# Performance work log

Measured on AMD Instinct MI355X. Metric: run time of the kernel, lower is better.

The kernel has to match this reference:

```python
import jax, jax.numpy as jnp
import numpy as np
import math

B, N, D_IN, D_MODEL, N_HEADS = 512, 1024, 8, 64, 4
SIG_DIM = D_IN + D_IN * D_IN  # sig_depth=2: 8 + 64 = 72


def setup_inputs() -> dict:
    key = jax.random.key(0)
    ks = jax.random.split(key, 16)
    s = 0.05
    inp = {
        "features": jax.random.normal(ks[0], (B, N, D_IN), dtype=jnp.float32),
        "W_sig": jax.random.normal(ks[1], (SIG_DIM, D_MODEL), dtype=jnp.float32) * s,
        "b_sig": jax.random.normal(ks[2], (D_MODEL,), dtype=jnp.float32) * s,
        "W_feat": jax.random.normal(ks[3], (D_IN + 1, D_MODEL), dtype=jnp.float32) * s,
        "b_feat": jax.random.normal(ks[4], (D_MODEL,), dtype=jnp.float32) * s,
        "W_q": jax.random.normal(ks[5], (D_MODEL, D_MODEL), dtype=jnp.float32) * s,
        "b_q": jax.random.normal(ks[6], (D_MODEL,), dtype=jnp.float32) * s,
        "W_k": jax.random.normal(ks[7], (D_MODEL, D_MODEL), dtype=jnp.float32) * s,
        "b_k": jax.random.normal(ks[8], (D_MODEL,), dtype=jnp.float32) * s,
        "W_v": jax.random.normal(ks[9], (D_MODEL, D_MODEL), dtype=jnp.float32) * s,
        "b_v": jax.random.normal(ks[10], (D_MODEL,), dtype=jnp.float32) * s,
        "W_o": jax.random.normal(ks[11], (D_MODEL, D_MODEL), dtype=jnp.float32) * s,
        "b_o": jax.random.normal(ks[12], (D_MODEL,), dtype=jnp.float32) * s,
        "W_out": jax.random.normal(ks[13], (D_MODEL, 1), dtype=jnp.float32) * s,
        "b_out": jax.random.normal(ks[14], (1,), dtype=jnp.float32) * s,
    }
    return inp


def reference(features, W_sig, b_sig, W_feat, b_feat, W_q, b_q, W_k, b_k,
              W_v, b_v, W_o, b_o, W_out, b_out):
    b, n, d = features.shape
    dm = W_sig.shape[1]
    dh = dm // N_HEADS
    dt = features.dtype

    # --- path signature (depth 2) for every prefix, via Chen/cumsum closed form ---
    # increments inc_t = f[t+1] - f[t], t = 0..n-2
    inc = features[:, 1:, :] - features[:, :-1, :]              # (b, n-1, d)
    # C_j = sum_{t<j} inc_t  (exclusive cumsum)
    C = jnp.cumsum(inc, axis=1) - inc                           # (b, n-1, d)
    # sum_{i<j} inc_i (x) inc_j, flattened row-major as in torch .view
    outer = (C[:, :, :, None] * inc[:, :, None, :]).reshape(b, n - 1, d * d)
    S2 = jnp.cumsum(outer, axis=1)                              # prefix k uses index k-1
    sig2 = jnp.concatenate([jnp.zeros((b, 1, d * d), dt), S2], axis=1)  # (b, n, d*d)
    sig1 = features - features[:, :1, :]                        # f[k] - f[0]
    sig = jnp.concatenate([sig1, sig2], axis=-1)                # (b, n, SIG_DIM)

    sig_feat = sig @ W_sig + b_sig                              # (b, n, dm)
    # step k=0 uses literal zeros (no projection, no bias) in the original
    sig_feat = sig_feat.at[:, 0, :].set(0.0)

    # --- cross-attn with single key/value: softmax weights are exactly 1 ---
    v = sig_feat @ W_v + b_v                                    # (b, n, dm)
    # deltas do not depend on the query path, so compute them first to break
    # the (vacuous) recurrence, then feed them back as prev_delta for q.
    deltas_pre = ((v @ W_o + b_o) @ W_out + b_out)[..., 0]      # (b, n)
    prev = jnp.concatenate([jnp.zeros((b, 1), dt), deltas_pre[:, :-1]], axis=1)

    x = jnp.concatenate([features, prev[:, :, None]], axis=-1) @ W_feat + b_feat
    q = x @ W_q + b_q
    k = sig_feat @ W_k + b_k

    qh = q.reshape(b, n, N_HEADS, dh)
    kh = k.reshape(b, n, N_HEADS, dh)
    vh = v.reshape(b, n, N_HEADS, dh)
    logits = (qh * kh).sum(-1, keepdims=True) / math.sqrt(dh)   # (b, n, H, 1)
    w = jax.nn.softmax(logits, axis=-1)                         # == 1 (single key)
    attn = (w * vh).reshape(b, n, dm)
    out = attn @ W_o + b_o
    deltas = (out @ W_out + b_out)[..., 0]                      # (b, n)
    return deltas
```

## Files before the change

kernel.cpp:

```cpp
#include <hip/hip_runtime.h>

#define NPOS 1024
#define D 8

__global__ void sig_prep(const float* __restrict__ W_sig, const float* __restrict__ b_sig,
                         const float* __restrict__ W_v,  const float* __restrict__ b_v,
                         const float* __restrict__ W_o,  const float* __restrict__ b_o,
                         const float* __restrict__ W_out,const float* __restrict__ b_out,
                         float* __restrict__ ws) {
    __shared__ float u1[64];
    __shared__ float u[64];
    const int tid = threadIdx.x;
    if (tid < 64) {
        float s = 0.f;
        for (int j = 0; j < 64; ++j) s += W_o[tid * 64 + j] * W_out[j];
        u1[tid] = s;
    }
    __syncthreads();
    if (tid < 64) {
        float s = 0.f;
        for (int j = 0; j < 64; ++j) s += W_v[tid * 64 + j] * u1[j];
        u[tid] = s;
    }
    __syncthreads();
    if (tid < 72) {
        float s = 0.f;
        for (int j = 0; j < 64; ++j) s += W_sig[tid * 64 + j] * u[j];
        ws[tid] = s;
    }
    if (tid == 72) {
        float c = b_out[0];
        for (int j = 0; j < 64; ++j) c += b_v[j] * u1[j] + b_o[j] * W_out[j];
        float dd = c;
        for (int j = 0; j < 64; ++j) dd += b_sig[j] * u[j];
        ws[72] = dd;
        ws[73] = c;
    }
}

__global__ __launch_bounds__(256) void sig_main(const float* __restrict__ feat,
                                                const float* __restrict__ ws,
                                                float* __restrict__ out) {
    __shared__ float w2s[64];
    __shared__ float w1s[8];
    __shared__ float wtot[4];

    const int tid = threadIdx.x;
    const int b   = blockIdx.x;

    if (tid < 64) w2s[tid] = ws[8 + tid];
    else if (tid < 72) w1s[tid - 64] = ws[tid - 64];
    const float dval = ws[72];
    const float cval = ws[73];

    const float* __restrict__ frow = feat + (size_t)b * NPOS * D;

    float f0[D];
    {
        float4 a0 = *reinterpret_cast<const float4*>(frow);
        float4 a1 = *reinterpret_cast<const float4*>(frow + 4);
        f0[0]=a0.x; f0[1]=a0.y; f0[2]=a0.z; f0[3]=a0.w;
        f0[4]=a1.x; f0[5]=a1.y; f0[6]=a1.z; f0[7]=a1.w;
    }

    const int a = tid * 4;
    float fp[D];
    {
        float4 p0 = *reinterpret_cast<const float4*>(frow + a * D);
        float4 p1 = *reinterpret_cast<const float4*>(frow + a * D + 4);
        fp[0]=p0.x; fp[1]=p0.y; fp[2]=p0.z; fp[3]=p0.w;
        fp[4]=p1.x; fp[5]=p1.y; fp[6]=p1.z; fp[7]=p1.w;
    }

    __syncthreads();

    float l[4];
    float dotv[4];
    float run = 0.f;
#pragma unroll
    for (int i = 0; i < 4; ++i) {
        const int s = a + i;
        float gi = 0.f;
        if (s < NPOS - 1) {
            float fn[D];
            float4 n0 = *reinterpret_cast<const float4*>(frow + (s + 1) * D);
            float4 n1 = *reinterpret_cast<const float4*>(frow + (s + 1) * D + 4);
            fn[0]=n0.x; fn[1]=n0.y; fn[2]=n0.z; fn[3]=n0.w;
            fn[4]=n1.x; fn[5]=n1.y; fn[6]=n1.z; fn[7]=n1.w;

            float inc[D];
#pragma unroll
            for (int k = 0; k < D; ++k) inc[k] = fn[k] - fp[k];
#pragma unroll
            for (int r = 0; r < D; ++r) {
                float acc = 0.f;
#pragma unroll
                for (int j = 0; j < D; ++j) acc += w2s[r * D + j] * inc[j];
                gi += (fp[r] - f0[r]) * acc;
            }
            float dv = 0.f;
#pragma unroll
            for (int k = 0; k < D; ++k) dv += (fn[k] - f0[k]) * w1s[k];
            dotv[i] = dv;
#pragma unroll
            for (int k = 0; k < D; ++k) fp[k] = fn[k];
        } else {
            dotv[i] = 0.f;
        }
        run += gi;
        l[i] = run;
    }

    const int lane = tid & 63;
    const int wave = tid >> 6;
    float t = run;
#pragma unroll
    for (int off = 1; off < 64; off <<= 1) {
        float nv = __shfl_up(t, off);
        if (lane >= off) t += nv;
    }
    if (lane == 63) wtot[wave] = t;
    __syncthreads();
    float base = t - run;
#pragma unroll
    for (int w = 0; w < 4; ++w)
        if (w < wave) base += wtot[w];

    float* __restrict__ orow = out + (size_t)b * NPOS;
    if (tid == 0) orow[0] = cval;
#pragma unroll
    for (int i = 0; i < 4; ++i) {
        const int s = a + i;
        const int tpos = s + 1;
        if (tpos < NPOS) {
            orow[tpos] = dotv[i] + base + l[i] + dval;
        }
    }
}

extern "C" void kernel_launch(void* const* d_in, const int* in_sizes, int n_in,
                              void* d_out, int out_size, void* d_ws, size_t ws_size,
                              hipStream_t stream) {
    const float* features = (const float*)d_in[0];
    const float* W_sig    = (const float*)d_in[1];
    const float* b_sig    = (const float*)d_in[2];
    const float* W_v      = (const float*)d_in[9];
    const float* b_v      = (const float*)d_in[10];
    const float* W_o      = (const float*)d_in[11];
    const float* b_o      = (const float*)d_in[12];
    const float* W_out    = (const float*)d_in[13];
    const float* b_out    = (const float*)d_in[14];

    float* ws  = (float*)d_ws;
    float* out = (float*)d_out;

    sig_prep<<<1, 128, 0, stream>>>(W_sig, b_sig, W_v, b_v, W_o, b_o, W_out, b_out, ws);
    sig_main<<<512, 256, 0, stream>>>(features, ws, out);
}
```

Measured before the change: 98.49 us.

## Fuse weight-prep into main kernel and use one thread per position

Drops the separate single-block prep kernel and has every block recompute the collapsed weight vectors (W_o·W_out, W_v·u, W_sig·u) into shared memory, saving a launch and the serial dependency between the two kernels. The main kernel moves from 256 threads doing 4 positions each to 1024 threads doing one position each, with a 16-wave scan instead of a 4-wave one. The cost is redundant 64x64 matrix-vector work in all 512 blocks, three extra barriers, and larger blocks.

```diff
diff --git a/kernel.cpp b/kernel.cpp
--- a/kernel.cpp
+++ b/kernel.cpp
@@ -3,59 +3,39 @@
 #define NPOS 1024
 #define D 8
 
-__global__ void sig_prep(const float* __restrict__ W_sig, const float* __restrict__ b_sig,
-                         const float* __restrict__ W_v,  const float* __restrict__ b_v,
-                         const float* __restrict__ W_o,  const float* __restrict__ b_o,
-                         const float* __restrict__ W_out,const float* __restrict__ b_out,
-                         float* __restrict__ ws) {
+__global__ __launch_bounds__(1024) void sig_fused(
+    const float* __restrict__ feat,
+    const float* __restrict__ W_sig, const float* __restrict__ b_sig,
+    const float* __restrict__ W_v,   const float* __restrict__ b_v,
+    const float* __restrict__ W_o,   const float* __restrict__ b_o,
+    const float* __restrict__ W_out, const float* __restrict__ b_out,
+    float* __restrict__ out)
+{
     __shared__ float u1[64];
-    __shared__ float u[64];
-    const int tid = threadIdx.x;
-    if (tid < 64) {
-        float s = 0.f;
-        for (int j = 0; j < 64; ++j) s += W_o[tid * 64 + j] * W_out[j];
-        u1[tid] = s;
-    }
-    __syncthreads();
-    if (tid < 64) {
-        float s = 0.f;
-        for (int j = 0; j < 64; ++j) s += W_v[tid * 64 + j] * u1[j];
-        u[tid] = s;
-    }
-    __syncthreads();
-    if (tid < 72) {
-        float s = 0.f;
-        for (int j = 0; j < 64; ++j) s += W_sig[tid * 64 + j] * u[j];
-        ws[tid] = s;
-    }
-    if (tid == 72) {
-        float c = b_out[0];
-        for (int j = 0; j < 64; ++j) c += b_v[j] * u1[j] + b_o[j] * W_out[j];
-        float dd = c;
-        for (int j = 0; j < 64; ++j) dd += b_sig[j] * u[j];
-        ws[72] = dd;
-        ws[73] = c;
-    }
-}
-
-__global__ __launch_bounds__(256) void sig_main(const float* __restrict__ feat,
-                                                const float* __restrict__ ws,
-                                                float* __restrict__ out) {
+    __shared__ float uu[64];
     __shared__ float w2s[64];
     __shared__ float w1s[8];
-    __shared__ float wtot[4];
+    __shared__ float dc[2];
+    __shared__ float wtot[16];
 
     const int tid = threadIdx.x;
     const int b   = blockIdx.x;
-
-    if (tid < 64) w2s[tid] = ws[8 + tid];
-    else if (tid < 72) w1s[tid - 64] = ws[tid - 64];
-    const float dval = ws[72];
-    const float cval = ws[73];
-
     const float* __restrict__ frow = feat + (size_t)b * NPOS * D;
 
-    float f0[D];
+    float fs[D], fn[D], f0[D];
+    {
+        float4 a0 = *reinterpret_cast<const float4*>(frow + tid * D);
+        float4 a1 = *reinterpret_cast<const float4*>(frow + tid * D + 4);
+        fs[0]=a0.x; fs[1]=a0.y; fs[2]=a0.z; fs[3]=a0.w;
+        fs[4]=a1.x; fs[5]=a1.y; fs[6]=a1.z; fs[7]=a1.w;
+    }
+    {
+        const int sn = (tid < NPOS - 1) ? (tid + 1) : tid;
+        float4 a0 = *reinterpret_cast<const float4*>(frow + sn * D);
+        float4 a1 = *reinterpret_cast<const float4*>(frow + sn * D + 4);
+        fn[0]=a0.x; fn[1]=a0.y; fn[2]=a0.z; fn[3]=a0.w;
+        fn[4]=a1.x; fn[5]=a1.y; fn[6]=a1.z; fn[7]=a1.w;
+    }
     {
         float4 a0 = *reinterpret_cast<const float4*>(frow);
         float4 a1 = *reinterpret_cast<const float4*>(frow + 4);
@@ -63,57 +43,58 @@
         f0[4]=a1.x; f0[5]=a1.y; f0[6]=a1.z; f0[7]=a1.w;
     }
 
-    const int a = tid * 4;
-    float fp[D];
-    {
-        float4 p0 = *reinterpret_cast<const float4*>(frow + a * D);
-        float4 p1 = *reinterpret_cast<const float4*>(frow + a * D + 4);
-        fp[0]=p0.x; fp[1]=p0.y; fp[2]=p0.z; fp[3]=p0.w;
-        fp[4]=p1.x; fp[5]=p1.y; fp[6]=p1.z; fp[7]=p1.w;
+    if (tid < 64) {
+        float s = 0.f;
+#pragma unroll
+        for (int j = 0; j < 64; ++j) s += W_o[tid * 64 + j] * W_out[j];
+        u1[tid] = s;
     }
-
+    __syncthreads();
+    if (tid < 64) {
+        float s = 0.f;
+#pragma unroll
+        for (int j = 0; j < 64; ++j) s += W_v[tid * 64 + j] * u1[j];
+        uu[tid] = s;
+    } else if (tid == 64) {
+        float c = b_out[0];
+#pragma unroll
+        for (int j = 0; j < 64; ++j) c += b_v[j] * u1[j] + b_o[j] * W_out[j];
+        dc[1] = c;
+    }
+    __syncthreads();
+    if (tid < 72) {
+        float s = 0.f;
+#pragma unroll
+        for (int j = 0; j < 64; ++j) s += W_sig[tid * 64 + j] * uu[j];
+        if (tid < 8) w1s[tid] = s;
+        else         w2s[tid - 8] = s;
+    } else if (tid == 72) {
+        float dd = dc[1];
+#pragma unroll
+        for (int j = 0; j < 64; ++j) dd += b_sig[j] * uu[j];
+        dc[0] = dd;
+    }
     __syncthreads();
 
-    float l[4];
-    float dotv[4];
-    float run = 0.f;
+    float gi = 0.f, dv = 0.f;
+    if (tid < NPOS - 1) {
+        float inc[D];
 #pragma unroll
-    for (int i = 0; i < 4; ++i) {
-        const int s = a + i;
-        float gi = 0.f;
-        if (s < NPOS - 1) {
-            float fn[D];
-            float4 n0 = *reinterpret_cast<const float4*>(frow + (s + 1) * D);
-            float4 n1 = *reinterpret_cast<const float4*>(frow + (s + 1) * D + 4);
-            fn[0]=n0.x; fn[1]=n0.y; fn[2]=n0.z; fn[3]=n0.w;
-            fn[4]=n1.x; fn[5]=n1.y; fn[6]=n1.z; fn[7]=n1.w;
-
-            float inc[D];
+        for (int k = 0; k < D; ++k) inc[k] = fn[k] - fs[k];
 #pragma unroll
-            for (int k = 0; k < D; ++k) inc[k] = fn[k] - fp[k];
+        for (int r = 0; r < D; ++r) {
+            float acc = 0.f;
 #pragma unroll
-            for (int r = 0; r < D; ++r) {
-                float acc = 0.f;
+            for (int j = 0; j < D; ++j) acc += w2s[r * D + j] * inc[j];
+            gi += (fs[r] - f0[r]) * acc;
+        }
 #pragma unroll
-                for (int j = 0; j < D; ++j) acc += w2s[r * D + j] * inc[j];
-                gi += (fp[r] - f0[r]) * acc;
-            }
-            float dv = 0.f;
-#pragma unroll
-            for (int k = 0; k < D; ++k) dv += (fn[k] - f0[k]) * w1s[k];
-            dotv[i] = dv;
-#pragma unroll
-            for (int k = 0; k < D; ++k) fp[k] = fn[k];
-        } else {
-            dotv[i] = 0.f;
-        }
-        run += gi;
-        l[i] = run;
+        for (int k = 0; k < D; ++k) dv += (fn[k] - f0[k]) * w1s[k];
     }
 
     const int lane = tid & 63;
     const int wave = tid >> 6;
-    float t = run;
+    float t = gi;
 #pragma unroll
     for (int off = 1; off < 64; off <<= 1) {
         float nv = __shfl_up(t, off);
@@ -121,21 +102,14 @@
     }
     if (lane == 63) wtot[wave] = t;
     __syncthreads();
-    float base = t - run;
+    float base = 0.f;
 #pragma unroll
-    for (int w = 0; w < 4; ++w)
+    for (int w = 0; w < 16; ++w)
         if (w < wave) base += wtot[w];
 
     float* __restrict__ orow = out + (size_t)b * NPOS;
-    if (tid == 0) orow[0] = cval;
-#pragma unroll
-    for (int i = 0; i < 4; ++i) {
-        const int s = a + i;
-        const int tpos = s + 1;
-        if (tpos < NPOS) {
-            orow[tpos] = dotv[i] + base + l[i] + dval;
-        }
-    }
+    if (tid == 0) orow[0] = dc[1];
+    if (tid < NPOS - 1) orow[tid + 1] = dv + base + t + dc[0];
 }
 
 extern "C" void kernel_launch(void* const* d_in, const int* in_sizes, int n_in,
@@ -151,9 +125,7 @@
     const float* W_out    = (const float*)d_in[13];
     const float* b_out    = (const float*)d_in[14];
 
-    float* ws  = (float*)d_ws;
-    float* out = (float*)d_out;
-
-    sig_prep<<<1, 128, 0, stream>>>(W_sig, b_sig, W_v, b_v, W_o, b_o, W_out, b_out, ws);
-    sig_main<<<512, 256, 0, stream>>>(features, ws, out);
+    float* o = (float*)d_out;
+    sig_fused<<<512, 1024, 0, stream>>>(features, W_sig, b_sig, W_v, b_v,
+                                        W_o, b_o, W_out, b_out, o);
 }
```

Result: no change. 96.72 us (-1.8%).
